# Kernel optimization log

Hardware: AMD Instinct MI355X
Metric: run time of the kernel (lower is better)

Reference implementation:

```python
import jax, jax.numpy as jnp
import numpy as np

WINDOW_SIZE = 7
C1 = 0.01 ** 2
C2 = 0.03 ** 2


def _gaussian_window(ws: int) -> jnp.ndarray:
    sigma = ws / 6.0
    coords = jnp.arange(ws, dtype=jnp.float32) - ws // 2
    g = jnp.exp(-coords ** 2 / (2 * sigma ** 2))
    g = g / g.sum()
    k3 = g[:, None, None] * g[None, :, None] * g[None, None, :]
    k3 = k3 / k3.sum()
    return k3.reshape(1, 1, ws, ws, ws)  # OIDHW


def _conv3d_same(x, w):
    pad = WINDOW_SIZE // 2
    return jax.lax.conv_general_dilated(
        x, w, window_strides=(1, 1, 1),
        padding=[(pad, pad)] * 3,
        dimension_numbers=('NCDHW', 'OIDHW', 'NCDHW'))


def setup_inputs() -> dict:
    key = jax.random.key(0)
    k1, k2 = jax.random.split(key)
    shape = (2, 1, 160, 160, 160)
    predicted = jax.random.uniform(k1, shape, dtype=jnp.float32)
    target = jax.random.uniform(k2, shape, dtype=jnp.float32)
    return {"predicted": predicted, "target": target}


def reference(predicted, target):
    window = _gaussian_window(WINDOW_SIZE)
    mu1 = _conv3d_same(predicted, window)
    mu2 = _conv3d_same(target, window)
    mu1_sq = mu1 ** 2
    mu2_sq = mu2 ** 2
    mu1_mu2 = mu1 * mu2
    sigma1_sq = _conv3d_same(predicted ** 2, window) - mu1_sq
    sigma2_sq = _conv3d_same(target ** 2, window) - mu2_sq
    sigma12 = _conv3d_same(predicted * target, window) - mu1_mu2
    ssim_map = ((2 * mu1_mu2 + C1) * (2 * sigma12 + C2)) / (
        (mu1_sq + mu2_sq + C1) * (sigma1_sq + sigma2_sq + C2))
    return 1.0 - ssim_map.mean()
```

## Files before the change

### kernel.cpp

```cpp
#include <hip/hip_runtime.h>
#include <math.h>

#define DD 160
#define HH 160
#define WW 160
#define NB 2
#define NEL (NB*DD*HH*WW)

#define XT 32
#define YT 16
#define ZC 16
#define NTHR 256
#define NZCH (DD/ZC)
#define GX (WW/XT)
#define GY (HH/YT)
#define NBLK (GX*GY*NB*NZCH)
#define NPART NBLK

#define HR 22
#define NJOB (HR*8)
#define CP 35

typedef float v2f __attribute__((ext_vector_type(2)));

struct G7 { float g[7]; };

__global__ __launch_bounds__(NTHR, 4) void ssim_fused(
        const float* __restrict__ p, const float* __restrict__ t,
        float* __restrict__ partial, G7 gw) {
    const int tid = threadIdx.x;
    const int tx  = tid & 31;
    const int tyo = tid >> 5;

    const int flat = blockIdx.x;
    const int w = (flat & 7) * (NBLK / 8) + (flat >> 3);
    const int bx = w % GX;
    const int by = (w / GX) % GY;
    const int bz = w / (GX * GY);

    const int x0 = bx * XT;
    const int y0 = by * YT;
    const int n  = bz / NZCH;
    const int zs = (bz % NZCH) * ZC;

    __shared__ float4 c4[2][HR][CP];

    v2f r01[2][6], r23[2][6];
#pragma unroll
    for (int yo = 0; yo < 2; ++yo)
#pragma unroll
        for (int j = 0; j < 6; ++j) {
            r01[yo][j] = (v2f)(0.f);
            r23[yo][j] = (v2f)(0.f);
        }

    const float C1v = 1e-4f, C2v = 9e-4f;
    float ssum = 0.f;
    const int hw = HH * WW;
    const float* pv = p + (size_t)n * DD * hw;
    const float* tv = t + (size_t)n * DD * hw;

    const int br = tid >> 3;
    const int bxg = tid & 7;
    const int bgy = y0 + br - 3;
    const bool browok = (unsigned)bgy < (unsigned)HH && tid < NJOB;
    const int cbase = x0 + 4 * bxg - 4;
    const int pcr = tx + (tx >> 3);

    float4 pfa[3], pfb[3];
    auto prefetch = [&](int sx) {
#pragma unroll
        for (int q = 0; q < 3; ++q) {
            pfa[q] = make_float4(0.f, 0.f, 0.f, 0.f);
            pfb[q] = make_float4(0.f, 0.f, 0.f, 0.f);
        }
        if (browok && sx >= 0 && sx < DD && sx < zs + ZC + 3) {
            const float* prow = pv + (size_t)sx * hw + bgy * WW;
            const float* trow = tv + (size_t)sx * hw + bgy * WW;
#pragma unroll
            for (int q = 0; q < 3; ++q) {
                int c0 = cbase + 4 * q;
                if ((unsigned)c0 < (unsigned)WW) {
                    pfa[q] = *(const float4*)(prow + c0);
                    pfb[q] = *(const float4*)(trow + c0);
                }
            }
        }
    };

    prefetch(zs - 3);

    for (int s = zs - 3; s < zs + ZC + 3; ++s) {
        const int par = s & 1;
        const bool valid = (s >= 0) && (s < DD);

        if (valid) {
            if (tid < NJOB) {
                v2f s01[4], s23[4];
#pragma unroll
                for (int e = 0; e < 4; ++e) { s01[e] = (v2f)(0.f); s23[e] = (v2f)(0.f); }
#pragma unroll
                for (int q = 0; q < 3; ++q) {
                    const float af[4] = {pfa[q].x, pfa[q].y, pfa[q].z, pfa[q].w};
                    const float bf[4] = {pfb[q].x, pfb[q].y, pfb[q].z, pfb[q].w};
#pragma unroll
                    for (int j = 0; j < 4; ++j) {
                        const int i = 4 * q + j;
                        v2f pt; pt[0] = af[j]; pt[1] = bf[j];
                        v2f ud; ud[0] = af[j] + bf[j]; ud[1] = af[j] - bf[j];
                        v2f qu = ud * ud;
#pragma unroll
                        for (int e = 0; e < 4; ++e) {
                            const int k = i - e - 1;
                            if (k >= 0 && k < 7) {
                                s01[e] = gw.g[k] * pt + s01[e];
                                s23[e] = gw.g[k] * qu + s23[e];
                            }
                        }
                    }
                }
#pragma unroll
                for (int e = 0; e < 4; ++e) {
                    int c = 4 * bxg + e;
                    c4[par][br][c + (c >> 3)] =
                        make_float4(s01[e][0], s01[e][1], s23[e][0], s23[e][1]);
                }
            }
            __syncthreads();
        }

        prefetch(s + 1);

        v2f m01[2], m23[2];
#pragma unroll
        for (int yo = 0; yo < 2; ++yo) {
            m01[yo] = (v2f)(0.f);
            m23[yo] = (v2f)(0.f);
        }

        if (valid) {
#pragma unroll
            for (int r8 = 0; r8 < 8; ++r8) {
                float4 v = c4[par][2 * tyo + r8][pcr];
                v2f v01; v01[0] = v.x; v01[1] = v.y;
                v2f v23; v23[0] = v.z; v23[1] = v.w;
                if (r8 < 7) {
                    float w2 = gw.g[r8];
                    m01[0] = w2 * v01 + m01[0];
                    m23[0] = w2 * v23 + m23[0];
                }
                if (r8 > 0) {
                    float w2 = gw.g[r8 - 1];
                    m01[1] = w2 * v01 + m01[1];
                    m23[1] = w2 * v23 + m23[1];
                }
            }
        }

#pragma unroll
        for (int yo = 0; yo < 2; ++yo) {
            v2f v01 = m01[yo], v23 = m23[yo];
            v2f cons01 = gw.g[6] * v01 + r01[yo][0];
            v2f cons23 = gw.g[6] * v23 + r23[yo][0];
#pragma unroll
            for (int j = 0; j < 5; ++j) {
                r01[yo][j] = gw.g[5 - j] * v01 + r01[yo][j + 1];
                r23[yo][j] = gw.g[5 - j] * v23 + r23[yo][j + 1];
            }
            r01[yo][5] = gw.g[0] * v01;
            r23[yo][5] = gw.g[0] * v23;

            if (s >= zs + 3) {
                float mu1 = cons01[0], mu2 = cons01[1];
                float Eu  = cons23[0], Ew  = cons23[1];
                float mu12 = mu1 * mu2, mu1sq = mu1 * mu1, mu2sq = mu2 * mu2;
                float sumsq = 0.5f  * (Eu + Ew) - mu1sq - mu2sq;
                float s12   = 0.25f * (Eu - Ew) - mu12;
                float num = (2.f * mu12 + C1v) * (2.f * s12 + C2v);
                float den = (mu1sq + mu2sq + C1v) * (sumsq + C2v);
                ssum += num * __builtin_amdgcn_rcpf(den);
            }
        }
    }

#pragma unroll
    for (int off = 32; off > 0; off >>= 1)
        ssum += __shfl_down(ssum, off, 64);
    __shared__ float wsum[4];
    if ((tid & 63) == 0) wsum[tid >> 6] = ssum;
    __syncthreads();
    if (tid == 0)
        partial[flat] = wsum[0] + wsum[1] + wsum[2] + wsum[3];
}

__global__ __launch_bounds__(256) void ssim_final(
        const float* __restrict__ partial, float* __restrict__ out) {
    float s = 0.f;
    for (int i = threadIdx.x; i < NPART; i += 256) s += partial[i];
#pragma unroll
    for (int off = 32; off > 0; off >>= 1)
        s += __shfl_down(s, off, 64);
    __shared__ float wsum[4];
    int lane = threadIdx.x & 63, wid = threadIdx.x >> 6;
    if (lane == 0) wsum[wid] = s;
    __syncthreads();
    if (threadIdx.x == 0) {
        float tot = wsum[0] + wsum[1] + wsum[2] + wsum[3];
        out[0] = 1.0f - tot / (float)NEL;
    }
}

extern "C" void kernel_launch(void* const* d_in, const int* in_sizes, int n_in,
                              void* d_out, int out_size, void* d_ws, size_t ws_size,
                              hipStream_t stream) {
    const float* p = (const float*)d_in[0];
    const float* t = (const float*)d_in[1];
    float* out = (float*)d_out;
    float* partial = (float*)d_ws;

    G7 gw;
    {
        double s = 0.0, sig = 7.0 / 6.0;
        double g[7];
        for (int i = 0; i < 7; ++i) {
            double d = (double)i - 3.0;
            g[i] = exp(-d * d / (2.0 * sig * sig));
            s += g[i];
        }
        for (int i = 0; i < 7; ++i) gw.g[i] = (float)(g[i] / s);
    }

    ssim_fused<<<NBLK, NTHR, 0, stream>>>(p, t, partial, gw);
    ssim_final<<<1, 256, 0, stream>>>(partial, out);
}
```

Before: 127.9 us.

## Give each wavefront a private halo tile to drop block-wide barriers

Splits the block's 16 output rows into four per-wave strips of 4 rows. Each wave computes its own 10-row x-convolved halo into a private shared-memory slice, so the block-wide __syncthreads becomes an intra-wave LDS wait. The register prefetch of the next slice is also removed, and loads now happen inline. In exchange, halo rows are recomputed redundantly across waves, roughly doubling the x-pass loads and FMAs, and the second halo pass runs with only 16 active lanes.

```diff
diff --git a/kernel.cpp b/kernel.cpp
--- a/kernel.cpp
+++ b/kernel.cpp
@@ -9,6 +9,7 @@
 
 #define XT 32
 #define YT 16
+#define YTW 4
 #define ZC 16
 #define NTHR 256
 #define NZCH (DD/ZC)
@@ -17,8 +18,7 @@
 #define NBLK (GX*GY*NB*NZCH)
 #define NPART NBLK
 
-#define HR 22
-#define NJOB (HR*8)
+#define WHR 10
 #define CP 35
 
 typedef float v2f __attribute__((ext_vector_type(2)));
@@ -28,9 +28,11 @@
 __global__ __launch_bounds__(NTHR, 4) void ssim_fused(
         const float* __restrict__ p, const float* __restrict__ t,
         float* __restrict__ partial, G7 gw) {
-    const int tid = threadIdx.x;
-    const int tx  = tid & 31;
-    const int tyo = tid >> 5;
+    const int tid  = threadIdx.x;
+    const int wid  = tid >> 6;
+    const int lane = tid & 63;
+    const int tx   = lane & 31;
+    const int tyo2 = lane >> 5;
 
     const int flat = blockIdx.x;
     const int w = (flat & 7) * (NBLK / 8) + (flat >> 3);
@@ -38,12 +40,12 @@
     const int by = (w / GX) % GY;
     const int bz = w / (GX * GY);
 
-    const int x0 = bx * XT;
-    const int y0 = by * YT;
-    const int n  = bz / NZCH;
-    const int zs = (bz % NZCH) * ZC;
-
-    __shared__ float4 c4[2][HR][CP];
+    const int x0  = bx * XT;
+    const int wy0 = by * YT + wid * YTW;
+    const int n   = bz / NZCH;
+    const int zs  = (bz % NZCH) * ZC;
+
+    __shared__ float4 xw[4][WHR][CP];
 
     v2f r01[2][6], r23[2][6];
 #pragma unroll
@@ -60,76 +62,79 @@
     const float* pv = p + (size_t)n * DD * hw;
     const float* tv = t + (size_t)n * DD * hw;
 
-    const int br = tid >> 3;
-    const int bxg = tid & 7;
-    const int bgy = y0 + br - 3;
-    const bool browok = (unsigned)bgy < (unsigned)HH && tid < NJOB;
-    const int cbase = x0 + 4 * bxg - 4;
+    const int wrA  = lane >> 3;
+    const int bxgA = lane & 7;
+    const int gyA  = wy0 + wrA - 3;
+    const bool gokA = (unsigned)gyA < (unsigned)HH;
+    const int cbA  = x0 + 4 * bxgA - 4;
+    bool qvA[3]; int qoffA[3];
+#pragma unroll
+    for (int q = 0; q < 3; ++q) {
+        const int c0 = cbA + 4 * q;
+        qvA[q] = gokA && ((unsigned)c0 < (unsigned)WW);
+        qoffA[q] = gyA * WW + c0;
+    }
+    const int cwsA = 4 * bxgA + (bxgA >> 1);
+
+    const bool hasB = lane < 16;
+    const int wrB  = 8 + (lane >> 3);
+    const int gyB  = wy0 + wrB - 3;
+    const bool gokB = hasB && ((unsigned)gyB < (unsigned)HH);
+    bool qvB[3]; int qoffB[3];
+#pragma unroll
+    for (int q = 0; q < 3; ++q) {
+        const int c0 = cbA + 4 * q;
+        qvB[q] = gokB && ((unsigned)c0 < (unsigned)WW);
+        qoffB[q] = gyB * WW + c0;
+    }
+
     const int pcr = tx + (tx >> 3);
 
-    float4 pfa[3], pfb[3];
-    auto prefetch = [&](int sx) {
+    auto xconv = [&](const float* ps, const float* ts,
+                     const bool (&qv)[3], const int (&qoff)[3],
+                     int wr, int cws) {
+        float4 A[3], Bv[3];
 #pragma unroll
         for (int q = 0; q < 3; ++q) {
-            pfa[q] = make_float4(0.f, 0.f, 0.f, 0.f);
-            pfb[q] = make_float4(0.f, 0.f, 0.f, 0.f);
-        }
-        if (browok && sx >= 0 && sx < DD && sx < zs + ZC + 3) {
-            const float* prow = pv + (size_t)sx * hw + bgy * WW;
-            const float* trow = tv + (size_t)sx * hw + bgy * WW;
-#pragma unroll
-            for (int q = 0; q < 3; ++q) {
-                int c0 = cbase + 4 * q;
-                if ((unsigned)c0 < (unsigned)WW) {
-                    pfa[q] = *(const float4*)(prow + c0);
-                    pfb[q] = *(const float4*)(trow + c0);
-                }
-            }
-        }
-    };
-
-    prefetch(zs - 3);
-
-    for (int s = zs - 3; s < zs + ZC + 3; ++s) {
-        const int par = s & 1;
-        const bool valid = (s >= 0) && (s < DD);
-
-        if (valid) {
-            if (tid < NJOB) {
-                v2f s01[4], s23[4];
-#pragma unroll
-                for (int e = 0; e < 4; ++e) { s01[e] = (v2f)(0.f); s23[e] = (v2f)(0.f); }
-#pragma unroll
-                for (int q = 0; q < 3; ++q) {
-                    const float af[4] = {pfa[q].x, pfa[q].y, pfa[q].z, pfa[q].w};
-                    const float bf[4] = {pfb[q].x, pfb[q].y, pfb[q].z, pfb[q].w};
-#pragma unroll
-                    for (int j = 0; j < 4; ++j) {
-                        const int i = 4 * q + j;
-                        v2f pt; pt[0] = af[j]; pt[1] = bf[j];
-                        v2f ud; ud[0] = af[j] + bf[j]; ud[1] = af[j] - bf[j];
-                        v2f qu = ud * ud;
-#pragma unroll
-                        for (int e = 0; e < 4; ++e) {
-                            const int k = i - e - 1;
-                            if (k >= 0 && k < 7) {
-                                s01[e] = gw.g[k] * pt + s01[e];
-                                s23[e] = gw.g[k] * qu + s23[e];
-                            }
-                        }
+            A[q]  = make_float4(0.f, 0.f, 0.f, 0.f);
+            Bv[q] = make_float4(0.f, 0.f, 0.f, 0.f);
+            if (qv[q]) {
+                A[q]  = *(const float4*)(ps + qoff[q]);
+                Bv[q] = *(const float4*)(ts + qoff[q]);
+            }
+        }
+        v2f s01[4], s23[4];
+#pragma unroll
+        for (int e = 0; e < 4; ++e) { s01[e] = (v2f)(0.f); s23[e] = (v2f)(0.f); }
+#pragma unroll
+        for (int q = 0; q < 3; ++q) {
+            const float af[4] = {A[q].x, A[q].y, A[q].z, A[q].w};
+            const float bf[4] = {Bv[q].x, Bv[q].y, Bv[q].z, Bv[q].w};
+#pragma unroll
+            for (int j = 0; j < 4; ++j) {
+                const int i = 4 * q + j;
+                v2f pt; pt[0] = af[j]; pt[1] = bf[j];
+                v2f ud; ud[0] = af[j] + bf[j]; ud[1] = af[j] - bf[j];
+                v2f qu = ud * ud;
+#pragma unroll
+                for (int e = 0; e < 4; ++e) {
+                    const int k = i - e - 1;
+                    if (k >= 0 && k < 7) {
+                        s01[e] = gw.g[k] * pt + s01[e];
+                        s23[e] = gw.g[k] * qu + s23[e];
                     }
                 }
-#pragma unroll
-                for (int e = 0; e < 4; ++e) {
-                    int c = 4 * bxg + e;
-                    c4[par][br][c + (c >> 3)] =
-                        make_float4(s01[e][0], s01[e][1], s23[e][0], s23[e][1]);
-                }
-            }
-            __syncthreads();
-        }
-
-        prefetch(s + 1);
+            }
+        }
+#pragma unroll
+        for (int e = 0; e < 4; ++e) {
+            xw[wid][wr][cws + e] =
+                make_float4(s01[e][0], s01[e][1], s23[e][0], s23[e][1]);
+        }
+    };
+
+    for (int s = zs - 3; s < zs + ZC + 3; ++s) {
+        const bool valid = (s >= 0) && (s < DD);
 
         v2f m01[2], m23[2];
 #pragma unroll
@@ -139,9 +144,18 @@
         }
 
         if (valid) {
+            const float* ps = pv + (size_t)s * hw;
+            const float* ts = tv + (size_t)s * hw;
+
+            xconv(ps, ts, qvA, qoffA, wrA, cwsA);
+            if (hasB)
+                xconv(ps, ts, qvB, qoffB, wrB, cwsA);
+            asm volatile("s_waitcnt lgkmcnt(0)" ::: "memory");
+
+            const float4* rbase = &xw[wid][2 * tyo2][pcr];
 #pragma unroll
             for (int r8 = 0; r8 < 8; ++r8) {
-                float4 v = c4[par][2 * tyo + r8][pcr];
+                float4 v = rbase[r8 * CP];
                 v2f v01; v01[0] = v.x; v01[1] = v.y;
                 v2f v23; v23[0] = v.z; v23[1] = v.w;
                 if (r8 < 7) {
```

New measurement: 160.4 us. +25.4%, slower.
